# Kernel optimization log

Measured on AMD Instinct MI355X. Metric: run time of the kernel, lower is better.

Reference implementation:

```python
import jax, jax.numpy as jnp
from jax import lax
import numpy as np

V, H, B, S = 32000, 1024, 32, 64


def setup_inputs() -> dict:
    key = jax.random.key(0)
    ks = jax.random.split(key, 10)
    scale = 0.02
    return {
        "encoder_output": jax.random.normal(ks[0], (B, S, H), dtype=jnp.float32),
        "encoder_hidden": jax.random.normal(ks[1], (1, B, H), dtype=jnp.float32),
        "bos_token": 1,
        "tgt_tensor": jax.random.randint(ks[2], (B, S), 0, V),
        "emb": jax.random.normal(ks[3], (V, H), dtype=jnp.float32) * scale,
        "W_ih": jax.random.normal(ks[4], (3 * H, H), dtype=jnp.float32) * scale,
        "W_hh": jax.random.normal(ks[5], (3 * H, H), dtype=jnp.float32) * scale,
        "b_ih": jnp.zeros((3 * H,), dtype=jnp.float32),
        "b_hh": jnp.zeros((3 * H,), dtype=jnp.float32),
        "W_out": jax.random.normal(ks[6], (V, H), dtype=jnp.float32) * scale,
        "b_out": jnp.zeros((V,), dtype=jnp.float32),
    }


def reference(encoder_output, encoder_hidden, bos_token, tgt_tensor,
              emb, W_ih, W_hh, b_ih, b_hh, W_out, b_out):
    Bb, Ss = encoder_output.shape[0], encoder_output.shape[1]
    # teacher forcing: input at step t is bos (t=0) then tgt[:, t-1]
    tokens = jnp.concatenate(
        [jnp.full((Bb, 1), bos_token, dtype=tgt_tensor.dtype), tgt_tensor[:, :-1]], axis=1)
    h0 = encoder_hidden[0]  # [B, H]

    def step(h, tok):
        x = jax.nn.relu(emb[tok])               # [B, H]
        gi = x @ W_ih.T + b_ih                  # [B, 3H]
        gh = h @ W_hh.T + b_hh                  # [B, 3H]
        ir, iz, in_ = jnp.split(gi, 3, axis=-1)
        hr, hz, hn = jnp.split(gh, 3, axis=-1)
        r = jax.nn.sigmoid(ir + hr)
        z = jax.nn.sigmoid(iz + hz)
        n = jnp.tanh(in_ + r * hn)
        h_new = (1.0 - z) * n + z * h
        return h_new, h_new

    hT, hs = lax.scan(step, h0, tokens.T)       # hs: [S, B, H]
    logits = jnp.einsum('sbh,vh->bsv', hs, W_out) + b_out  # [B, S, V]
    log_probs = jax.nn.log_softmax(logits, axis=-1)
    return log_probs, hT[None]
```

## Files before the change

kernel.cpp:

```cpp
#include <hip/hip_runtime.h>

typedef unsigned short ushort_t;
typedef __attribute__((ext_vector_type(4)))  float f32x4;
typedef __attribute__((ext_vector_type(16))) float f32x16;
typedef __attribute__((ext_vector_type(8)))  short s16x8;
typedef __attribute__((ext_vector_type(4)))  short s16x4;

#define AS1C(p) ((const __attribute__((address_space(1))) void*)(p))
#define AS3(p)  ((__attribute__((address_space(3))) void*)(p))

#define VV 32000
#define HH 1024
#define BB 32
#define SS 64

__device__ __forceinline__ ushort_t f2bf(float f){
  unsigned u = __builtin_bit_cast(unsigned, f);
  unsigned r = u + 0x7fffu + ((u >> 16) & 1u);
  return (ushort_t)(r >> 16);
}

__global__ __launch_bounds__(256) void k_f32_to_bf16(const float* __restrict__ src,
                                                     ushort_t* __restrict__ dst, int n4){
  int i = blockIdx.x * 256 + threadIdx.x;
  if (i >= n4) return;
  f32x4 v = *(const f32x4*)(src + (size_t)i * 4);
  s16x4 o;
  #pragma unroll
  for (int j = 0; j < 4; j++) o[j] = (short)f2bf(v[j]);
  *(s16x4*)(dst + (size_t)i * 4) = o;
}

__global__ __launch_bounds__(256) void k_embed(const float* __restrict__ emb,
                                               const int* __restrict__ tgt,
                                               const int* __restrict__ bosp,
                                               ushort_t* __restrict__ xb){
  int r = blockIdx.x;
  int s = r >> 5, b = r & 31;
  int tok = (s == 0) ? bosp[0] : tgt[b * SS + (s - 1)];
  const float* src = emb + (size_t)tok * HH;
  ushort_t* dst = xb + (size_t)r * HH;
  int k4 = threadIdx.x * 4;
  f32x4 v = *(const f32x4*)(src + k4);
  s16x4 o;
  #pragma unroll
  for (int j = 0; j < 4; j++){ float x = v[j]; x = x > 0.f ? x : 0.f; o[j] = (short)f2bf(x); }
  *(s16x4*)(dst + k4) = o;
}

__global__ __launch_bounds__(256) void k_gemm_bt(const ushort_t* __restrict__ A,
                                                 const ushort_t* __restrict__ Bw,
                                                 const float* __restrict__ bias,
                                                 float* __restrict__ C,
                                                 int M, int N, int K, int permute){
  __shared__ ushort_t sA[128 * 32];
  __shared__ ushort_t sB[128 * 32];
  int m0 = blockIdx.x * 128;
  int n0 = blockIdx.y * 128;
  int tid = threadIdx.x;
  int lane = tid & 63, wave = tid >> 6;
  int wm = (wave >> 1) * 64, wn = (wave & 1) * 64;
  int l16 = lane & 15, quad = lane >> 4;
  f32x4 acc[4][4] = {};
  for (int k0 = 0; k0 < K; k0 += 32){
    #pragma unroll
    for (int i = 0; i < 2; i++){
      int id = tid + i * 256;
      int row = id >> 2, kc = id & 3;
      __builtin_amdgcn_global_load_lds(AS1C(A + (size_t)(m0 + row) * K + k0 + kc * 8),
                                       AS3(sA + (size_t)id * 8), 16, 0, 0);
      __builtin_amdgcn_global_load_lds(AS1C(Bw + (size_t)(n0 + row) * K + k0 + kc * 8),
                                       AS3(sB + (size_t)id * 8), 16, 0, 0);
    }
    __syncthreads();
    s16x8 af[4], bf[4];
    #pragma unroll
    for (int t = 0; t < 4; t++){
      af[t] = *(const s16x8*)(sA + (wm + t * 16 + l16) * 32 + quad * 8);
      bf[t] = *(const s16x8*)(sB + (wn + t * 16 + l16) * 32 + quad * 8);
    }
    #pragma unroll
    for (int mt = 0; mt < 4; mt++)
      #pragma unroll
      for (int nt = 0; nt < 4; nt++)
        acc[mt][nt] = __builtin_amdgcn_mfma_f32_16x16x32_bf16(af[mt], bf[nt], acc[mt][nt], 0, 0, 0);
    __syncthreads();
  }
  #pragma unroll
  for (int nt = 0; nt < 4; nt++){
    int col = n0 + wn + nt * 16 + l16;
    float bs = bias ? bias[col] : 0.f;
    #pragma unroll
    for (int mt = 0; mt < 4; mt++){
      #pragma unroll
      for (int r = 0; r < 4; r++){
        int row = m0 + wm + mt * 16 + quad * 4 + r;
        int orow = permute ? ((row & 31) * SS + (row >> 5)) : row;
        C[(size_t)orow * N + col] = acc[mt][nt][r] + bs;
      }
    }
  }
}

__global__ __launch_bounds__(256) void k_gru_step(const ushort_t* __restrict__ hprev_bf,
                                                  const float* __restrict__ hprev_f,
                                                  const ushort_t* __restrict__ Whh,
                                                  const float* __restrict__ gi_s,
                                                  const float* __restrict__ b_hh,
                                                  ushort_t* __restrict__ hout_bf,
                                                  float* __restrict__ hout_f){
  int tid = threadIdx.x;
  int lane = tid & 63, wave = tid >> 6;
  int j0 = blockIdx.x * 32;
  int m = lane & 31, q = lane >> 5;
  int kbase = wave * 256;
  f32x16 acc0 = {}, acc1 = {}, acc2 = {};
  const ushort_t* arow = hprev_bf + (size_t)m * HH + kbase + q * 8;
  const ushort_t* b0 = Whh + (size_t)(0 * HH + j0 + m) * HH + kbase + q * 8;
  const ushort_t* b1 = Whh + (size_t)(1 * HH + j0 + m) * HH + kbase + q * 8;
  const ushort_t* b2 = Whh + (size_t)(2 * HH + j0 + m) * HH + kbase + q * 8;
  #pragma unroll
  for (int kk = 0; kk < 256; kk += 16){
    s16x8 a = *(const s16x8*)(arow + kk);
    acc0 = __builtin_amdgcn_mfma_f32_32x32x16_bf16(a, *(const s16x8*)(b0 + kk), acc0, 0, 0, 0);
    acc1 = __builtin_amdgcn_mfma_f32_32x32x16_bf16(a, *(const s16x8*)(b1 + kk), acc1, 0, 0, 0);
    acc2 = __builtin_amdgcn_mfma_f32_32x32x16_bf16(a, *(const s16x8*)(b2 + kk), acc2, 0, 0, 0);
  }
  __shared__ float red[4][3][1024];
  #pragma unroll
  for (int r = 0; r < 16; r++){
    int row = (r & 3) + 8 * (r >> 2) + 4 * q;
    red[wave][0][row * 32 + m] = acc0[r];
    red[wave][1][row * 32 + m] = acc1[r];
    red[wave][2][row * 32 + m] = acc2[r];
  }
  __syncthreads();
  #pragma unroll
  for (int i = 0; i < 4; i++){
    int e = tid + i * 256;
    int b = e >> 5, j = e & 31;
    int jj = j0 + j;
    float hr = red[0][0][e] + red[1][0][e] + red[2][0][e] + red[3][0][e] + b_hh[jj];
    float hz = red[0][1][e] + red[1][1][e] + red[2][1][e] + red[3][1][e] + b_hh[HH + jj];
    float hn = red[0][2][e] + red[1][2][e] + red[2][2][e] + red[3][2][e] + b_hh[2 * HH + jj];
    const float* gib = gi_s + (size_t)b * (3 * HH);
    float r_ = 1.f / (1.f + __expf(-(gib[jj] + hr)));
    float z_ = 1.f / (1.f + __expf(-(gib[HH + jj] + hz)));
    float n_ = tanhf(gib[2 * HH + jj] + r_ * hn);
    float hp = hprev_f[b * HH + jj];
    float hv = (1.f - z_) * n_ + z_ * hp;
    hout_f[b * HH + jj] = hv;
    hout_bf[b * HH + jj] = f2bf(hv);
  }
}

__global__ __launch_bounds__(256) void k_logsoftmax(float* __restrict__ out){
  float* p = out + (size_t)blockIdx.x * VV;
  int tid = threadIdx.x;
  float m = -3.0e38f, l = 0.f;
  for (int i = tid; i < VV; i += 256){
    float x = p[i];
    float mn = fmaxf(m, x);
    l = l * __expf(m - mn) + __expf(x - mn);
    m = mn;
  }
  #pragma unroll
  for (int off = 32; off; off >>= 1){
    float mo = __shfl_down(m, off);
    float lo = __shfl_down(l, off);
    float mn = fmaxf(m, mo);
    l = l * __expf(m - mn) + lo * __expf(mo - mn);
    m = mn;
  }
  __shared__ float sm[4], sl[4];
  int w = tid >> 6;
  if ((tid & 63) == 0){ sm[w] = m; sl[w] = l; }
  __syncthreads();
  float M = fmaxf(fmaxf(sm[0], sm[1]), fmaxf(sm[2], sm[3]));
  float L = sl[0] * __expf(sm[0] - M) + sl[1] * __expf(sm[1] - M)
          + sl[2] * __expf(sm[2] - M) + sl[3] * __expf(sm[3] - M);
  float off = M + __logf(L);
  for (int i = tid; i < VV; i += 256) p[i] -= off;
}

__global__ __launch_bounds__(256) void k_copy(const float* __restrict__ src,
                                              float* __restrict__ dst, int n){
  int i = blockIdx.x * 256 + threadIdx.x;
  if (i < n) dst[i] = src[i];
}

extern "C" void kernel_launch(void* const* d_in, const int* in_sizes, int n_in,
                              void* d_out, int out_size, void* d_ws, size_t ws_size,
                              hipStream_t stream){
  const float* enc_hid = (const float*)d_in[1];
  const int*   bosp    = (const int*)d_in[2];
  const int*   tgt     = (const int*)d_in[3];
  const float* emb     = (const float*)d_in[4];
  const float* W_ih    = (const float*)d_in[5];
  const float* W_hh    = (const float*)d_in[6];
  const float* b_ih    = (const float*)d_in[7];
  const float* b_hh    = (const float*)d_in[8];
  const float* W_out   = (const float*)d_in[9];
  const float* b_out   = (const float*)d_in[10];
  float* out = (float*)d_out;

  const size_t NWOUT = (size_t)VV * HH;
  const size_t NW3H  = (size_t)3 * HH * HH;
  const size_t NX    = (size_t)SS * BB * HH;
  const size_t NH0   = (size_t)BB * HH;
  const size_t NGI   = (size_t)SS * BB * 3 * HH;
  ushort_t* wout_bf = (ushort_t*)d_ws;
  ushort_t* wih_bf  = wout_bf + NWOUT;
  ushort_t* whh_bf  = wih_bf + NW3H;
  ushort_t* x_bf    = whh_bf + NW3H;
  ushort_t* h0_bf   = x_bf + NX;
  ushort_t* hs_bf   = h0_bf + NH0;
  float*    gi      = (float*)(hs_bf + NX);
  float*    hs_f    = gi + NGI;

  k_f32_to_bf16<<<(int)((NWOUT/4 + 255)/256), 256, 0, stream>>>(W_out, wout_bf, (int)(NWOUT/4));
  k_f32_to_bf16<<<(int)((NW3H/4  + 255)/256), 256, 0, stream>>>(W_ih,  wih_bf,  (int)(NW3H/4));
  k_f32_to_bf16<<<(int)((NW3H/4  + 255)/256), 256, 0, stream>>>(W_hh,  whh_bf,  (int)(NW3H/4));
  k_f32_to_bf16<<<(int)((NH0/4   + 255)/256), 256, 0, stream>>>(enc_hid, h0_bf, (int)(NH0/4));

  k_embed<<<SS*BB, 256, 0, stream>>>(emb, tgt, bosp, x_bf);

  k_gemm_bt<<<dim3(16, 24), 256, 0, stream>>>(x_bf, wih_bf, b_ih, gi, 2048, 3072, 1024, 0);

  for (int s = 0; s < SS; s++){
    const ushort_t* hp_bf = s ? hs_bf + (size_t)(s - 1) * NH0 : h0_bf;
    const float*    hp_f  = s ? hs_f + (size_t)(s - 1) * NH0 : enc_hid;
    k_gru_step<<<32, 256, 0, stream>>>(hp_bf, hp_f, whh_bf,
                                       gi + (size_t)s * BB * 3 * HH, b_hh,
                                       hs_bf + (size_t)s * NH0,
                                       hs_f + (size_t)s * NH0);
  }

  k_copy<<<(int)((NH0 + 255)/256), 256, 0, stream>>>(hs_f + (size_t)63 * NH0,
                                                     out + (size_t)BB * SS * VV, (int)NH0);

  k_gemm_bt<<<dim3(16, 250), 256, 0, stream>>>(hs_bf, wout_bf, b_out, out, 2048, VV, 1024, 1);

  k_logsoftmax<<<SS*BB, 256, 0, stream>>>(out);
}
```

Measured before the change: 1.622 ms.

## Replace per-step GRU launches with persistent grid-barrier kernel; store intermediates in bf16

The 64 separate GRU step launches become one persistent kernel of 64 workgroups. Each workgroup keeps its 16-column slice of W_hh in LDS and keeps the fp32 hidden state in registers. Steps synchronize through a global atomic barrier, which removes per-step launch overhead and repeated W_hh reads from memory. The input-gate projection and, when the workspace is large enough, the output logits are written in bf16, and a new log-softmax reads the bf16 logits through LDS. This cuts memory traffic but loses precision in the logits and gates, and the spin barrier relies on all 64 workgroups being co-resident.

New measurement: 1.411 ms. -13.0%, faster.

```diff
diff --git a/kernel.cpp b/kernel.cpp
--- a/kernel.cpp
+++ b/kernel.cpp
@@ -2,7 +2,6 @@
 
 typedef unsigned short ushort_t;
 typedef __attribute__((ext_vector_type(4)))  float f32x4;
-typedef __attribute__((ext_vector_type(16))) float f32x16;
 typedef __attribute__((ext_vector_type(8)))  short s16x8;
 typedef __attribute__((ext_vector_type(4)))  short s16x4;
 
@@ -13,11 +12,16 @@
 #define HH 1024
 #define BB 32
 #define SS 64
+#define GRU_WGS 64
 
 __device__ __forceinline__ ushort_t f2bf(float f){
   unsigned u = __builtin_bit_cast(unsigned, f);
   unsigned r = u + 0x7fffu + ((u >> 16) & 1u);
   return (ushort_t)(r >> 16);
+}
+__device__ __forceinline__ float bf2f(ushort_t u){
+  unsigned x = ((unsigned)u) << 16;
+  return __builtin_bit_cast(float, x);
 }
 
 __global__ __launch_bounds__(256) void k_f32_to_bf16(const float* __restrict__ src,
@@ -48,10 +52,11 @@
   *(s16x4*)(dst + k4) = o;
 }
 
+template<bool BF16OUT>
 __global__ __launch_bounds__(256) void k_gemm_bt(const ushort_t* __restrict__ A,
                                                  const ushort_t* __restrict__ Bw,
                                                  const float* __restrict__ bias,
-                                                 float* __restrict__ C,
+                                                 void* __restrict__ Cv,
                                                  int M, int N, int K, int permute){
   __shared__ ushort_t sA[128 * 32];
   __shared__ ushort_t sB[128 * 32];
@@ -96,61 +101,143 @@
       for (int r = 0; r < 4; r++){
         int row = m0 + wm + mt * 16 + quad * 4 + r;
         int orow = permute ? ((row & 31) * SS + (row >> 5)) : row;
-        C[(size_t)orow * N + col] = acc[mt][nt][r] + bs;
+        float v = acc[mt][nt][r] + bs;
+        if (BF16OUT) ((ushort_t*)Cv)[(size_t)orow * N + col] = f2bf(v);
+        else         ((float*)Cv)[(size_t)orow * N + col] = v;
       }
     }
   }
 }
 
-__global__ __launch_bounds__(256) void k_gru_step(const ushort_t* __restrict__ hprev_bf,
-                                                  const float* __restrict__ hprev_f,
-                                                  const ushort_t* __restrict__ Whh,
-                                                  const float* __restrict__ gi_s,
-                                                  const float* __restrict__ b_hh,
-                                                  ushort_t* __restrict__ hout_bf,
-                                                  float* __restrict__ hout_f){
+__global__ __launch_bounds__(256) void k_gru_persist(
+    const ushort_t* __restrict__ h0_bf, const float* __restrict__ h0_f,
+    const ushort_t* __restrict__ Whh,
+    const ushort_t* __restrict__ gi,
+    const float* __restrict__ b_hh,
+    ushort_t* __restrict__ hs_bf,
+    float* __restrict__ hT,
+    unsigned* __restrict__ bar){
+  __shared__ ushort_t sW[3][16][1032];
+  __shared__ float red[4][3][32][17];
   int tid = threadIdx.x;
+  int wg = blockIdx.x;
+  int j0 = wg * 16;
   int lane = tid & 63, wave = tid >> 6;
-  int j0 = blockIdx.x * 32;
-  int m = lane & 31, q = lane >> 5;
-  int kbase = wave * 256;
-  f32x16 acc0 = {}, acc1 = {}, acc2 = {};
-  const ushort_t* arow = hprev_bf + (size_t)m * HH + kbase + q * 8;
-  const ushort_t* b0 = Whh + (size_t)(0 * HH + j0 + m) * HH + kbase + q * 8;
-  const ushort_t* b1 = Whh + (size_t)(1 * HH + j0 + m) * HH + kbase + q * 8;
-  const ushort_t* b2 = Whh + (size_t)(2 * HH + j0 + m) * HH + kbase + q * 8;
-  #pragma unroll
-  for (int kk = 0; kk < 256; kk += 16){
-    s16x8 a = *(const s16x8*)(arow + kk);
-    acc0 = __builtin_amdgcn_mfma_f32_32x32x16_bf16(a, *(const s16x8*)(b0 + kk), acc0, 0, 0, 0);
-    acc1 = __builtin_amdgcn_mfma_f32_32x32x16_bf16(a, *(const s16x8*)(b1 + kk), acc1, 0, 0, 0);
-    acc2 = __builtin_amdgcn_mfma_f32_32x32x16_bf16(a, *(const s16x8*)(b2 + kk), acc2, 0, 0, 0);
-  }
-  __shared__ float red[4][3][1024];
-  #pragma unroll
-  for (int r = 0; r < 16; r++){
-    int row = (r & 3) + 8 * (r >> 2) + 4 * q;
-    red[wave][0][row * 32 + m] = acc0[r];
-    red[wave][1][row * 32 + m] = acc1[r];
-    red[wave][2][row * 32 + m] = acc2[r];
+  int l16 = lane & 15, quad = lane >> 4;
+
+  for (int idx = tid; idx < 48 * 128; idx += 256){
+    int row = idx >> 7, c = idx & 127;
+    *(s16x8*)&sW[row >> 4][row & 15][c * 8] =
+        *(const s16x8*)(Whh + (size_t)((row >> 4) * HH + j0 + (row & 15)) * HH + c * 8);
+  }
+  float hreg[2]; float bh[2][3];
+  #pragma unroll
+  for (int i = 0; i < 2; i++){
+    int e = tid + i * 256, b = e >> 4, jj = e & 15;
+    hreg[i] = h0_f[b * HH + j0 + jj];
+    bh[i][0] = b_hh[j0 + jj];
+    bh[i][1] = b_hh[HH + j0 + jj];
+    bh[i][2] = b_hh[2 * HH + j0 + jj];
   }
   __syncthreads();
-  #pragma unroll
-  for (int i = 0; i < 4; i++){
-    int e = tid + i * 256;
-    int b = e >> 5, j = e & 31;
-    int jj = j0 + j;
-    float hr = red[0][0][e] + red[1][0][e] + red[2][0][e] + red[3][0][e] + b_hh[jj];
-    float hz = red[0][1][e] + red[1][1][e] + red[2][1][e] + red[3][1][e] + b_hh[HH + jj];
-    float hn = red[0][2][e] + red[1][2][e] + red[2][2][e] + red[3][2][e] + b_hh[2 * HH + jj];
-    const float* gib = gi_s + (size_t)b * (3 * HH);
-    float r_ = 1.f / (1.f + __expf(-(gib[jj] + hr)));
-    float z_ = 1.f / (1.f + __expf(-(gib[HH + jj] + hz)));
-    float n_ = tanhf(gib[2 * HH + jj] + r_ * hn);
-    float hp = hprev_f[b * HH + jj];
-    float hv = (1.f - z_) * n_ + z_ * hp;
-    hout_f[b * HH + jj] = hv;
-    hout_bf[b * HH + jj] = f2bf(hv);
+
+  int kb = wave * 256;
+  for (int s = 0; s < SS; s++){
+    const ushort_t* hp = s ? (hs_bf + (size_t)(s - 1) * BB * HH) : h0_bf;
+    f32x4 acc[3][2] = {};
+    #pragma unroll
+    for (int kk = 0; kk < 8; kk++){
+      int ko = kb + kk * 32 + quad * 8;
+      s16x8 a0 = *(const s16x8*)(hp + (size_t)l16 * HH + ko);
+      s16x8 a1 = *(const s16x8*)(hp + (size_t)(16 + l16) * HH + ko);
+      #pragma unroll
+      for (int g = 0; g < 3; g++){
+        s16x8 bfr = *(const s16x8*)&sW[g][l16][ko];
+        acc[g][0] = __builtin_amdgcn_mfma_f32_16x16x32_bf16(a0, bfr, acc[g][0], 0, 0, 0);
+        acc[g][1] = __builtin_amdgcn_mfma_f32_16x16x32_bf16(a1, bfr, acc[g][1], 0, 0, 0);
+      }
+    }
+    #pragma unroll
+    for (int g = 0; g < 3; g++)
+      #pragma unroll
+      for (int mh = 0; mh < 2; mh++)
+        #pragma unroll
+        for (int r = 0; r < 4; r++)
+          red[wave][g][mh * 16 + quad * 4 + r][l16] = acc[g][mh][r];
+    __syncthreads();
+    ushort_t* ho = hs_bf + (size_t)s * BB * HH;
+    #pragma unroll
+    for (int i = 0; i < 2; i++){
+      int e = tid + i * 256, b = e >> 4, jj = e & 15;
+      float hr = red[0][0][b][jj] + red[1][0][b][jj] + red[2][0][b][jj] + red[3][0][b][jj] + bh[i][0];
+      float hz = red[0][1][b][jj] + red[1][1][b][jj] + red[2][1][b][jj] + red[3][1][b][jj] + bh[i][1];
+      float hn = red[0][2][b][jj] + red[1][2][b][jj] + red[2][2][b][jj] + red[3][2][b][jj] + bh[i][2];
+      const ushort_t* gib = gi + (size_t)s * BB * 3 * HH + (size_t)b * 3 * HH;
+      float r_ = 1.f / (1.f + __expf(-(bf2f(gib[j0 + jj]) + hr)));
+      float z_ = 1.f / (1.f + __expf(-(bf2f(gib[HH + j0 + jj]) + hz)));
+      float n_ = tanhf(bf2f(gib[2 * HH + j0 + jj]) + r_ * hn);
+      float hv = (1.f - z_) * n_ + z_ * hreg[i];
+      hreg[i] = hv;
+      ho[b * HH + j0 + jj] = f2bf(hv);
+    }
+    __threadfence();
+    __syncthreads();
+    if (tid == 0){
+      __hip_atomic_fetch_add(bar, 1u, __ATOMIC_ACQ_REL, __HIP_MEMORY_SCOPE_AGENT);
+      unsigned tgt = (unsigned)(s + 1) * GRU_WGS;
+      while (__hip_atomic_load(bar, __ATOMIC_ACQUIRE, __HIP_MEMORY_SCOPE_AGENT) < tgt)
+        __builtin_amdgcn_s_sleep(4);
+    }
+    __syncthreads();
+  }
+  #pragma unroll
+  for (int i = 0; i < 2; i++){
+    int e = tid + i * 256, b = e >> 4, jj = e & 15;
+    hT[b * HH + j0 + jj] = hreg[i];
+  }
+}
+
+__global__ __launch_bounds__(256) void k_lsm_bf(const ushort_t* __restrict__ lg,
+                                                float* __restrict__ out){
+  __shared__ ushort_t srow[VV];
+  __shared__ float sm[4], sl[4];
+  const ushort_t* p = lg + (size_t)blockIdx.x * VV;
+  float* q = out + (size_t)blockIdx.x * VV;
+  int tid = threadIdx.x;
+  float m = -3.0e38f, l = 0.f;
+  for (int c = tid; c < VV / 8; c += 256){
+    s16x8 v = *(const s16x8*)(p + c * 8);
+    *(s16x8*)(srow + c * 8) = v;
+    #pragma unroll
+    for (int j = 0; j < 8; j++){
+      float x = bf2f((ushort_t)v[j]);
+      float mn = fmaxf(m, x);
+      l = l * __expf(m - mn) + __expf(x - mn);
+      m = mn;
+    }
+  }
+  #pragma unroll
+  for (int off = 32; off; off >>= 1){
+    float mo = __shfl_down(m, off);
+    float lo = __shfl_down(l, off);
+    float mn = fmaxf(m, mo);
+    l = l * __expf(m - mn) + lo * __expf(mo - mn);
+    m = mn;
+  }
+  int w = tid >> 6;
+  if ((tid & 63) == 0){ sm[w] = m; sl[w] = l; }
+  __syncthreads();
+  float M = fmaxf(fmaxf(sm[0], sm[1]), fmaxf(sm[2], sm[3]));
+  float L = sl[0] * __expf(sm[0] - M) + sl[1] * __expf(sm[1] - M)
+          + sl[2] * __expf(sm[2] - M) + sl[3] * __expf(sm[3] - M);
+  float off = M + __logf(L);
+  for (int c = tid; c < VV / 8; c += 256){
+    s16x8 v = *(const s16x8*)(srow + c * 8);
+    f32x4 o0, o1;
+    #pragma unroll
+    for (int j = 0; j < 4; j++){ o0[j] = bf2f((ushort_t)v[j]) - off; o1[j] = bf2f((ushort_t)v[4 + j]) - off; }
+    *(f32x4*)(q + c * 8) = o0;
+    *(f32x4*)(q + c * 8 + 4) = o1;
   }
 }
 
@@ -181,12 +268,6 @@
           + sl[2] * __expf(sm[2] - M) + sl[3] * __expf(sm[3] - M);
   float off = M + __logf(L);
   for (int i = tid; i < VV; i += 256) p[i] -= off;
-}
-
-__global__ __launch_bounds__(256) void k_copy(const float* __restrict__ src,
-                                              float* __restrict__ dst, int n){
-  int i = blockIdx.x * 256 + threadIdx.x;
-  if (i < n) dst[i] = src[i];
 }
 
 extern "C" void kernel_launch(void* const* d_in, const int* in_sizes, int n_in,
@@ -209,14 +290,18 @@
   const size_t NX    = (size_t)SS * BB * HH;
   const size_t NH0   = (size_t)BB * HH;
   const size_t NGI   = (size_t)SS * BB * 3 * HH;
-  ushort_t* wout_bf = (ushort_t*)d_ws;
-  ushort_t* wih_bf  = wout_bf + NWOUT;
-  ushort_t* whh_bf  = wih_bf + NW3H;
-  ushort_t* x_bf    = whh_bf + NW3H;
-  ushort_t* h0_bf   = x_bf + NX;
-  ushort_t* hs_bf   = h0_bf + NH0;
-  float*    gi      = (float*)(hs_bf + NX);
-  float*    hs_f    = gi + NGI;
+  char* wp = (char*)d_ws;
+  ushort_t* wout_bf = (ushort_t*)wp;               wp += NWOUT * 2;
+  ushort_t* wih_bf  = (ushort_t*)wp;               wp += NW3H * 2;
+  ushort_t* whh_bf  = (ushort_t*)wp;               wp += NW3H * 2;
+  ushort_t* x_bf    = (ushort_t*)wp;               wp += NX * 2;
+  ushort_t* h0_bf   = (ushort_t*)wp;               wp += NH0 * 2;
+  ushort_t* hs_bf   = (ushort_t*)wp;               wp += NX * 2;
+  ushort_t* gi_bf   = (ushort_t*)wp;               wp += NGI * 2;
+  unsigned* bar     = (unsigned*)wp;               wp += 16;
+  ushort_t* logits_bf = (ushort_t*)wp;
+  size_t need_big = (size_t)(wp - (char*)d_ws) + (size_t)BB * SS * VV * 2 + 1024;
+  bool big = ws_size >= need_big;
 
   k_f32_to_bf16<<<(int)((NWOUT/4 + 255)/256), 256, 0, stream>>>(W_out, wout_bf, (int)(NWOUT/4));
   k_f32_to_bf16<<<(int)((NW3H/4  + 255)/256), 256, 0, stream>>>(W_ih,  wih_bf,  (int)(NW3H/4));
@@ -225,21 +310,19 @@
 
   k_embed<<<SS*BB, 256, 0, stream>>>(emb, tgt, bosp, x_bf);
 
-  k_gemm_bt<<<dim3(16, 24), 256, 0, stream>>>(x_bf, wih_bf, b_ih, gi, 2048, 3072, 1024, 0);
-
-  for (int s = 0; s < SS; s++){
-    const ushort_t* hp_bf = s ? hs_bf + (size_t)(s - 1) * NH0 : h0_bf;
-    const float*    hp_f  = s ? hs_f + (size_t)(s - 1) * NH0 : enc_hid;
-    k_gru_step<<<32, 256, 0, stream>>>(hp_bf, hp_f, whh_bf,
-                                       gi + (size_t)s * BB * 3 * HH, b_hh,
-                                       hs_bf + (size_t)s * NH0,
-                                       hs_f + (size_t)s * NH0);
-  }
-
-  k_copy<<<(int)((NH0 + 255)/256), 256, 0, stream>>>(hs_f + (size_t)63 * NH0,
-                                                     out + (size_t)BB * SS * VV, (int)NH0);
-
-  k_gemm_bt<<<dim3(16, 250), 256, 0, stream>>>(hs_bf, wout_bf, b_out, out, 2048, VV, 1024, 1);
-
-  k_logsoftmax<<<SS*BB, 256, 0, stream>>>(out);
-}
+  k_gemm_bt<true><<<dim3(16, 24), 256, 0, stream>>>(x_bf, wih_bf, b_ih, gi_bf, 2048, 3072, 1024, 0);
+
+  hipMemsetAsync(bar, 0, 4, stream);
+  k_gru_persist<<<GRU_WGS, 256, 0, stream>>>(h0_bf, enc_hid, whh_bf, gi_bf, b_hh,
+                                             hs_bf, out + (size_t)BB * SS * VV, bar);
+
+  if (big){
+    k_gemm_bt<true><<<dim3(16, 250), 256, 0, stream>>>(hs_bf, wout_bf, b_out, logits_bf,
+                                                       2048, VV, 1024, 1);
+    k_lsm_bf<<<SS*BB, 256, 0, stream>>>(logits_bf, out);
+  } else {
+    k_gemm_bt<false><<<dim3(16, 250), 256, 0, stream>>>(hs_bf, wout_bf, b_out, out,
+                                                        2048, VV, 1024, 1);
+    k_logsoftmax<<<SS*BB, 256, 0, stream>>>(out);
+  }
+}
```
